# Optimization experiments

Measured on AMD Instinct MI355X. Metric: run time of the kernel, lower is better.

## Reference

```python
import jax, jax.numpy as jnp
import numpy as np

N_TOKENS = 100000
CUT = [0, 20000, 50000, 100000]  # cutoff_ends
D = 1024


def setup_inputs() -> dict:
    key = jax.random.key(0)
    ks = jax.random.split(key, 12)
    B, S = 2, 1024
    hidden = jax.random.normal(ks[0], (B, S, D), dtype=jnp.float32)
    target = jax.random.randint(ks[1], (B, S), 0, N_TOKENS, dtype=jnp.int64)
    s = 0.02
    # cluster 0 (shortlist) + cluster projection head
    w0 = jax.random.normal(ks[2], (20000, 1024), dtype=jnp.float32) * s
    b0 = jnp.zeros((20000,), jnp.float32)
    cluster_w = jax.random.normal(ks[3], (2, 1024), dtype=jnp.float32) * s  # n_clusters=2
    cluster_b = jnp.zeros((2,), jnp.float32)
    proj0 = jax.random.normal(ks[4], (1024, 1024), dtype=jnp.float32) * s  # d_proj x d_emb_0
    # tail cluster 1: d_emb_1 = 1024 // 4 = 256, vocab slice 20000..50000
    w1 = jax.random.normal(ks[5], (30000, 256), dtype=jnp.float32) * s
    b1 = jnp.zeros((30000,), jnp.float32)
    proj1 = jax.random.normal(ks[6], (1024, 256), dtype=jnp.float32) * s
    # tail cluster 2: d_emb_2 = 1024 // 16 = 64, vocab slice 50000..100000
    w2 = jax.random.normal(ks[7], (50000, 64), dtype=jnp.float32) * s
    b2 = jnp.zeros((50000,), jnp.float32)
    proj2 = jax.random.normal(ks[8], (1024, 64), dtype=jnp.float32) * s
    return {"hidden": hidden, "target": target,
            "w0": w0, "b0": b0, "cluster_w": cluster_w, "cluster_b": cluster_b, "proj0": proj0,
            "w1": w1, "b1": b1, "proj1": proj1,
            "w2": w2, "b2": b2, "proj2": proj2}


def reference(hidden, target, w0, b0, cluster_w, cluster_b, proj0,
              w1, b1, proj1, w2, b2, proj2):
    tgt_shape = target.shape
    h = hidden.reshape(-1, D)            # [N, d_proj]
    t = target.reshape(-1)               # [N]

    # head: shortlist logits + cluster logits, via low-rank projection
    head_w = jnp.concatenate([w0, cluster_w], axis=0)   # [20002, 1024]
    head_b = jnp.concatenate([b0, cluster_b], axis=0)
    head_logit = (h @ proj0) @ head_w.T + head_b        # [N, 20002]
    head_lp = jax.nn.log_softmax(head_logit, axis=1)

    nll = jnp.zeros(t.shape, h.dtype)

    # cluster 0 (shortlist): logprob is head_lp at the target id
    m0 = t < CUT[1]
    idx0 = jnp.clip(t, 0, CUT[1] - 1)
    lp0 = jnp.take_along_axis(head_lp, idx0[:, None], axis=1)[:, 0]
    nll = jnp.where(m0, -lp0, nll)

    # tail clusters. NOTE: faithful to original quirk head_logprob[:, -i]
    tails = [(CUT[1], CUT[2], w1, b1, proj1), (CUT[2], CUT[3], w2, b2, proj2)]
    for i, (left, right, w, b, p) in enumerate(tails, start=1):
        m = (t >= left) & (t < right)
        tail_logit = (h @ p) @ w.T + b                  # [N, right-left]
        tail_lp = jax.nn.log_softmax(tail_logit, axis=1)
        ti = jnp.clip(t - left, 0, right - left - 1)
        lp = head_lp[:, -i] + jnp.take_along_axis(tail_lp, ti[:, None], axis=1)[:, 0]
        nll = jnp.where(m, -lp, nll)

    return nll.reshape(tgt_shape)
```

## Files before the change

kernel.cpp:

```cpp
#include <hip/hip_runtime.h>
#include <cstdint>
#include <cstddef>

#define DEV static __device__ __forceinline__

typedef __attribute__((ext_vector_type(8))) short bf16x8_t;
typedef __attribute__((ext_vector_type(4))) float f32x4_t;

DEV unsigned short f2bf(float f) {
  union { float f; unsigned u; } v; v.f = f;
  unsigned r = v.u + 0x7fffu + ((v.u >> 16) & 1u);
  return (unsigned short)(r >> 16);
}

DEV void gl_lds16(const void* g, void* l) {
  __builtin_amdgcn_global_load_lds(
      (const __attribute__((address_space(1))) void*)g,
      (__attribute__((address_space(3))) void*)l,
      16, 0, 0);
}

__global__ __launch_bounds__(256)
void prep_k(const int* __restrict__ target,
            int* __restrict__ idx1, int* __restrict__ pos1,
            int* __restrict__ idx2, int* __restrict__ pos2,
            int* __restrict__ cnts,
            const float* __restrict__ p0, const float* __restrict__ p1,
            const float* __restrict__ p2, unsigned short* __restrict__ pAll,
            const float* __restrict__ s0, unsigned short* __restrict__ d0, int n0,
            const float* __restrict__ s1, unsigned short* __restrict__ d1, int n1,
            const float* __restrict__ s2, unsigned short* __restrict__ d2, int n2,
            const float* __restrict__ s3, unsigned short* __restrict__ d3, int n3,
            const float* __restrict__ s4, unsigned short* __restrict__ d4, int n4) {
  const int bid = blockIdx.x;
  const int tid = threadIdx.x;
  if (bid == 0) {
    __shared__ int c1, c2;
    if (tid == 0) { c1 = 0; c2 = 0; }
    __syncthreads();
    for (int i = tid; i < 2048; i += 256) {
      int t = target[i];
      if (t >= 20000 && t < 50000) {
        int p = atomicAdd(&c1, 1); idx1[p] = i; pos1[i] = p;
      } else if (t >= 50000) {
        int p = atomicAdd(&c2, 1); idx2[p] = i; pos2[i] = p;
      }
    }
    __syncthreads();
    if (tid == 0) { cnts[0] = c1; cnts[1] = c2; }
    return;
  }
  if (bid <= 1344) {
    __shared__ float tile[32][33];
    int b = bid - 1;
    const float* src; unsigned short* dst; int C, bx, by;
    if (b < 1024)      { src = p0; dst = pAll;               C = 1024; bx = b % 32; by = b / 32; }
    else if (b < 1280) { int q = b - 1024; src = p1; dst = pAll + 1024 * 1024; C = 256; bx = q % 8; by = q / 8; }
    else               { int q = b - 1280; src = p2; dst = pAll + 1280 * 1024; C = 64;  bx = q % 2; by = q / 2; }
    const int R = 1024;
    int tx = tid & 31, ty = tid >> 5;
    int c0 = bx * 32, r0 = by * 32;
    for (int yy = ty; yy < 32; yy += 8)
      tile[yy][tx] = src[(size_t)(r0 + yy) * C + (c0 + tx)];
    __syncthreads();
    for (int yy = ty; yy < 32; yy += 8)
      dst[(size_t)(c0 + yy) * R + (r0 + tx)] = f2bf(tile[tx][yy]);
    return;
  }
  int j = (bid - 1345) * 256 + tid;
  const float* s; unsigned short* d;
  if (j < n0) { s = s0; d = d0; }
  else { j -= n0;
    if (j < n1) { s = s1; d = d1; }
    else { j -= n1;
      if (j < n2) { s = s2; d = d2; }
      else { j -= n2;
        if (j < n3) { s = s3; d = d3; }
        else { j -= n3; if (j >= n4) return; s = s4; d = d4; }
      }
    }
  }
  float4 f = ((const float4*)s)[j];
  ushort4 o;
  o.x = f2bf(f.x); o.y = f2bf(f.y); o.z = f2bf(f.z); o.w = f2bf(f.w);
  ((ushort4*)d)[j] = o;
}

__global__ __launch_bounds__(256)
void proj_gemm_k(const unsigned short* __restrict__ A,
                 const unsigned short* __restrict__ W,
                 unsigned short* __restrict__ Cout) {
  __shared__ __align__(16) unsigned short As[128 * 32];
  __shared__ __align__(16) unsigned short Bs[128 * 32];
  const int K = 1024, V = 1344;
  const int tm = blockIdx.x, tn = blockIdx.y;
  const int m0 = tm * 128, n0 = tn * 128;
  const int tid = threadIdx.x, wid = tid >> 6, lane = tid & 63;
  const int quad = lane >> 4, l16 = lane & 15;
  const int wr = wid >> 1, wc = wid & 1;

  f32x4_t acc[4][4];
  const f32x4_t zero4 = {0.f, 0.f, 0.f, 0.f};
#pragma unroll
  for (int i = 0; i < 4; ++i)
#pragma unroll
    for (int j = 0; j < 4; ++j) acc[i][j] = zero4;

  const int srow = wid * 32 + (lane >> 2);
  const int skk  = (lane & 3) * 8;
  const unsigned short* Ap0 = A + (size_t)(m0 + srow) * K + skk;
  const unsigned short* Ap1 = A + (size_t)(m0 + srow + 16) * K + skk;
  int wrow0 = n0 + srow;      if (wrow0 > V - 1) wrow0 = V - 1;
  int wrow1 = n0 + srow + 16; if (wrow1 > V - 1) wrow1 = V - 1;
  const unsigned short* Wp0 = W + (size_t)wrow0 * K + skk;
  const unsigned short* Wp1 = W + (size_t)wrow1 * K + skk;
  unsigned short* Asw = As + wid * 1024;
  unsigned short* Bsw = Bs + wid * 1024;

  for (int k0 = 0; k0 < K; k0 += 32) {
    gl_lds16(Ap0, Asw);
    gl_lds16(Ap1, Asw + 512);
    gl_lds16(Wp0, Bsw);
    gl_lds16(Wp1, Bsw + 512);
    Ap0 += 32; Ap1 += 32; Wp0 += 32; Wp1 += 32;
    __syncthreads();
    bf16x8_t af[4], bfr[4];
#pragma unroll
    for (int i = 0; i < 4; ++i)
      af[i] = *(const bf16x8_t*)(As + (size_t)(wr * 64 + i * 16 + l16) * 32 + quad * 8);
#pragma unroll
    for (int j = 0; j < 4; ++j)
      bfr[j] = *(const bf16x8_t*)(Bs + (size_t)(wc * 64 + j * 16 + l16) * 32 + quad * 8);
#pragma unroll
    for (int i = 0; i < 4; ++i)
#pragma unroll
      for (int j = 0; j < 4; ++j)
        acc[i][j] = __builtin_amdgcn_mfma_f32_16x16x32_bf16(af[i], bfr[j], acc[i][j], 0, 0, 0);
    __syncthreads();
  }
#pragma unroll
  for (int i = 0; i < 4; ++i)
#pragma unroll
    for (int j = 0; j < 4; ++j) {
      const int n = n0 + wc * 64 + j * 16 + l16;
      if (n < V) {
#pragma unroll
        for (int r = 0; r < 4; ++r) {
          const int m = m0 + wr * 64 + i * 16 + quad * 4 + r;
          Cout[(size_t)m * V + n] = f2bf(acc[i][j][r]);
        }
      }
    }
}


#define SBAR() __builtin_amdgcn_s_barrier()

#define STA(BUF, HALF, KT)                                                    \
  {                                                                           \
    const unsigned short* g_ = aB0 + (size_t)(HALF) * (128 * 1344) + (KT) * 64; \
    char* d_ = (char*)SA[BUF][HALF] + ldsw;                                   \
    gl_lds16(g_, d_);                                                         \
    gl_lds16(g_ + 64 * 1344, d_ + 8192);                                      \
  }

#define STB(BUF, HALF, KT)                                                    \
  {                                                                           \
    char* d_ = (char*)SB[BUF][HALF] + ldsw;                                   \
    gl_lds16(bP##HALF##0 + (KT) * 64, d_);                                    \
    gl_lds16(bP##HALF##1 + (KT) * 64, d_ + 8192);                             \
  }

#define MMQ(mb, nb, BB)                                                       \
  {                                                                           \
    _Pragma("unroll") for (int mi = 0; mi < 4; ++mi) {                        \
      _Pragma("unroll") for (int nj = 0; nj < 2; ++nj) {                      \
        acc[(mb) + mi][(nb) + nj] = __builtin_amdgcn_mfma_f32_16x16x32_bf16(  \
            Af[0][mi], BB[0][nj], acc[(mb) + mi][(nb) + nj], 0, 0, 0);        \
        acc[(mb) + mi][(nb) + nj] = __builtin_amdgcn_mfma_f32_16x16x32_bf16(  \
            Af[1][mi], BB[1][nj], acc[(mb) + mi][(nb) + nj], 0, 0, 0);        \
      }                                                                       \
    }                                                                         \
  }

#define PH(D_, E_, KTV)                                                       \
  {                                                                           \
    const int kt_ = (KTV);                                                    \
    const int t1_ = (kt_ + 1 > 15) ? 15 : (kt_ + 1);                          \
    const int t2_ = (kt_ + 2 > 15) ? 15 : (kt_ + 2);                          \
              \
    _Pragma("unroll") for (int mi = 0; mi < 4; ++mi) {                        \
      Af[0][mi] = *(const bf16x8_t*)(pa##D_##a + mi * 2048);                  \
      Af[1][mi] = *(const bf16x8_t*)(pa##D_##b + mi * 2048);                  \
    }                                                                         \
    _Pragma("unroll") for (int nj = 0; nj < 2; ++nj) {                        \
      Bh[0][nj] = *(const bf16x8_t*)(pb##D_##a + (2 + nj) * 2048);            \
      Bh[1][nj] = *(const bf16x8_t*)(pb##D_##b + (2 + nj) * 2048);            \
    }                                                                         \
    STB(E_, 1, t1_);                                                          \
    __builtin_amdgcn_s_setprio(1); MMQ(0, 0, Bl); __builtin_amdgcn_s_setprio(0); \
    SBAR();                                                                   \
              \
    __builtin_amdgcn_s_setprio(1); MMQ(0, 2, Bh); __builtin_amdgcn_s_setprio(0); \
    _Pragma("unroll") for (int mi = 0; mi < 4; ++mi) {                        \
      Af[0][mi] = *(const bf16x8_t*)(pa##D_##a + (4 + mi) * 2048);            \
      Af[1][mi] = *(const bf16x8_t*)(pa##D_##b + (4 + mi) * 2048);            \
    }                                                                         \
    STA(E_, 1, t1_);                                                          \
    SBAR();                                                                   \
               \
    STB(D_, 0, t2_);                                                          \
    __builtin_amdgcn_s_setprio(1); MMQ(4, 0, Bl); __builtin_amdgcn_s_setprio(0); \
    asm volatile("s_waitcnt vmcnt(2)" ::: "memory");                          \
    SBAR();                                                                   \
           \
    STA(D_, 0, t2_);                                                          \
    _Pragma("unroll") for (int nj = 0; nj < 2; ++nj) {                        \
      Bl[0][nj] = *(const bf16x8_t*)(pb##E_##a + nj * 2048);                  \
      Bl[1][nj] = *(const bf16x8_t*)(pb##E_##b + nj * 2048);                  \
    }                                                                         \
    __builtin_amdgcn_s_setprio(1); MMQ(4, 2, Bh); __builtin_amdgcn_s_setprio(0); \
    SBAR();                                                                   \
  }

#define PROLOGUE6()                                                           \
  { STB(0, 0, 0); STA(0, 0, 0); STB(0, 1, 0); STA(0, 1, 0);                   \
    STB(1, 0, 1); STA(1, 0, 1); }

typedef unsigned short lds_half_t[2][8192];

DEV void head_body(char* UB, int bid,
                   const unsigned short* __restrict__ Pall,
                   const unsigned short* __restrict__ w0b,
                   const float* __restrict__ b0, const float* __restrict__ cb,
                   float* __restrict__ part0, float* __restrict__ g0,
                   float* __restrict__ cg, const int* __restrict__ target) {
  lds_half_t* SA = (lds_half_t*)UB;
  lds_half_t* SB = (lds_half_t*)(UB + 65536);

  const int V = 20002;
  const int orig = (bid & 7) * 79 + (bid >> 3);
  const int mt = orig & 7, stripe = orig >> 3;
  const int m0 = mt * 256, n0 = stripe * 256;

  const int tid = threadIdx.x;
  const int wid = tid >> 6, lane = tid & 63;
  const int quad = lane >> 4, l16 = lane & 15;
  const int wr = wid >> 2, wc = wid & 3;

  const int r0  = tid >> 3;
  const int ibh = ((tid & 7) ^ (r0 & 7)) << 3;

  const unsigned short* aB0 = Pall + (size_t)(m0 + r0) * 1344 + ibh;
  int br00 = n0 + r0;            if (br00 > V - 1) br00 = V - 1;
  int br01 = n0 + r0 + 64;       if (br01 > V - 1) br01 = V - 1;
  int br10 = n0 + 128 + r0;      if (br10 > V - 1) br10 = V - 1;
  int br11 = n0 + 128 + r0 + 64; if (br11 > V - 1) br11 = V - 1;
  const unsigned short* bP00 = w0b + (size_t)br00 * 1024 + ibh;
  const unsigned short* bP01 = w0b + (size_t)br01 * 1024 + ibh;
  const unsigned short* bP10 = w0b + (size_t)br10 * 1024 + ibh;
  const unsigned short* bP11 = w0b + (size_t)br11 * 1024 + ibh;

  const int ldsw = wid * 1024;

  const int aoff0 = l16 * 128 + ((quad ^ (l16 & 3)) << 4) + (((l16 >> 2) & 1) << 6);
  const int aoff1 = aoff0 ^ 64;
  const char* pa0a = (const char*)SA[0][wr] + aoff0;
  const char* pa0b = (const char*)SA[0][wr] + aoff1;
  const char* pa1a = (const char*)SA[1][wr] + aoff0;
  const char* pa1b = (const char*)SA[1][wr] + aoff1;
  const char* pb0a = (const char*)SB[0][wc >> 1] + (wc & 1) * 8192 + aoff0;
  const char* pb0b = (const char*)SB[0][wc >> 1] + (wc & 1) * 8192 + aoff1;
  const char* pb1a = (const char*)SB[1][wc >> 1] + (wc & 1) * 8192 + aoff0;
  const char* pb1b = (const char*)SB[1][wc >> 1] + (wc & 1) * 8192 + aoff1;

  f32x4_t acc[8][4];
  const f32x4_t zero4 = {0.f, 0.f, 0.f, 0.f};
#pragma unroll
  for (int i = 0; i < 8; ++i)
#pragma unroll
    for (int j = 0; j < 4; ++j) acc[i][j] = zero4;

  bf16x8_t Af[2][4];
  bf16x8_t Bl[2][2];
  bf16x8_t Bh[2][2];

  PROLOGUE6();
  asm volatile("s_waitcnt vmcnt(4)" ::: "memory");
  SBAR();
#pragma unroll
  for (int nj = 0; nj < 2; ++nj) {
    Bl[0][nj] = *(const bf16x8_t*)(pb0a + nj * 2048);
    Bl[1][nj] = *(const bf16x8_t*)(pb0b + nj * 2048);
  }

#pragma unroll 1
  for (int ktp = 0; ktp < 8; ++ktp) {
    const int kt0 = 2 * ktp;
    PH(0, 1, kt0);
    PH(1, 0, kt0 + 1);
  }

  asm volatile("s_waitcnt vmcnt(0) lgkmcnt(0)" ::: "memory");
  SBAR();

  int nj[4]; float bj[4];
#pragma unroll
  for (int j = 0; j < 4; ++j) {
    nj[j] = n0 + wc * 64 + j * 16 + l16;
    bj[j] = (nj[j] < 20000) ? b0[nj[j]] : ((nj[j] < V) ? cb[nj[j] - 20000] : 0.f);
  }
  float* redf = (float*)UB;
#pragma unroll
  for (int i = 0; i < 8; ++i) {
#pragma unroll
    for (int r = 0; r < 4; ++r) {
      const int rloc = i * 16 + quad * 4 + r;
      const int token = m0 + wr * 128 + rloc;
      float v[4], sum = 0.f;
#pragma unroll
      for (int j = 0; j < 4; ++j) {
        v[j] = acc[i][j][r] + bj[j];
        if (nj[j] < V) sum += __expf(v[j]);
      }
#pragma unroll
      for (int off = 1; off < 16; off <<= 1)
        sum += __shfl_xor(sum, off, 64);
      if (l16 == 0) redf[(wr * 4 + wc) * 128 + rloc] = sum;
      const int t = target[token];
      const int gi = (t < 19999) ? t : 19999;
#pragma unroll
      for (int j = 0; j < 4; ++j) {
        if (nj[j] == gi) g0[token] = v[j];
        if (nj[j] == 20000) cg[2 * token]     = v[j];
        if (nj[j] == 20001) cg[2 * token + 1] = v[j];
      }
    }
  }
  __syncthreads();
  if (tid < 256) {
    const int wrr = tid >> 7, rr = tid & 127;
    const float s = redf[(wrr * 4 + 0) * 128 + rr] + redf[(wrr * 4 + 1) * 128 + rr]
                  + redf[(wrr * 4 + 2) * 128 + rr] + redf[(wrr * 4 + 3) * 128 + rr];
    part0[(size_t)(m0 + tid) * 79 + stripe] = s;
  }
}

#undef PH
#undef MMQ
#undef STA
#undef STB
#undef PROLOGUE6
#undef SBAR

template <int KT>
DEV void tail_body(char* UB, int tn,
                   const unsigned short* __restrict__ A, int ldA,
                   const unsigned short* __restrict__ W,
                   const float* __restrict__ bias, int V, int ntiles,
                   const int* __restrict__ rowidx,
                   const int* __restrict__ cnt_ptr,
                   float* __restrict__ partials,
                   float* __restrict__ gathered,
                   const int* __restrict__ target, int glo) {
  constexpr int NC = KT / 32;
  unsigned short (*Ws)[128 * 32] = (unsigned short (*)[128 * 32])UB;
  unsigned short (*As)[128 * 32] = (unsigned short (*)[128 * 32])(UB + NC * 8192);
  float (*red)[128] = (float (*)[128])(UB + 2 * NC * 8192);

  const int n0 = tn * 128;
  const int Meff = *cnt_ptr;
  const int tid = threadIdx.x;
  const bool act = tid < 256;
  const int wid = tid >> 6, lane = tid & 63;
  const int quad = lane >> 4, l16 = lane & 15;
  const int wr = wid >> 1, wc = wid & 1;
  const int srow = wid * 32 + (lane >> 2);
  const int skk  = (lane & 3) * 8;

  int wrow0 = n0 + srow;      if (wrow0 > V - 1) wrow0 = V - 1;
  int wrow1 = n0 + srow + 16; if (wrow1 > V - 1) wrow1 = V - 1;
  if (act) {
#pragma unroll
    for (int c = 0; c < NC; ++c) {
      gl_lds16(W + (size_t)wrow0 * KT + c * 32 + skk, Ws[c] + wid * 1024);
      gl_lds16(W + (size_t)wrow1 * KT + c * 32 + skk, Ws[c] + wid * 1024 + 512);
    }
  }

  int nj[4]; float bj[4];
#pragma unroll
  for (int j = 0; j < 4; ++j) {
    nj[j] = n0 + wc * 64 + j * 16 + l16;
    bj[j] = (act && nj[j] < V) ? bias[nj[j]] : 0.f;
  }

  const int nm = (Meff + 127) >> 7;
  for (int m = 0; m < nm; ++m) {
    const int m0 = m * 128;
    if (act) {
      int ar0 = m0 + srow;      if (ar0 > Meff - 1) ar0 = Meff - 1;
      int ar1 = m0 + srow + 16; if (ar1 > Meff - 1) ar1 = Meff - 1;
      ar0 = rowidx[ar0]; ar1 = rowidx[ar1];
#pragma unroll
      for (int c = 0; c < NC; ++c) {
        gl_lds16(A + (size_t)ar0 * ldA + c * 32 + skk, As[c] + wid * 1024);
        gl_lds16(A + (size_t)ar1 * ldA + c * 32 + skk, As[c] + wid * 1024 + 512);
      }
    }
    __syncthreads();

    if (act) {
      f32x4_t acc[4][4];
      const f32x4_t zero4 = {0.f, 0.f, 0.f, 0.f};
#pragma unroll
      for (int i = 0; i < 4; ++i)
#pragma unroll
        for (int j = 0; j < 4; ++j) acc[i][j] = zero4;
#pragma unroll
      for (int c = 0; c < NC; ++c) {
        bf16x8_t af[4], bfr[4];
#pragma unroll
        for (int i = 0; i < 4; ++i)
          af[i] = *(const bf16x8_t*)(As[c] + (size_t)(wr * 64 + i * 16 + l16) * 32 + quad * 8);
#pragma unroll
        for (int j = 0; j < 4; ++j)
          bfr[j] = *(const bf16x8_t*)(Ws[c] + (size_t)(wc * 64 + j * 16 + l16) * 32 + quad * 8);
#pragma unroll
        for (int i = 0; i < 4; ++i)
#pragma unroll
          for (int j = 0; j < 4; ++j)
            acc[i][j] = __builtin_amdgcn_mfma_f32_16x16x32_bf16(af[i], bfr[j], acc[i][j], 0, 0, 0);
      }

#pragma unroll
      for (int i = 0; i < 4; ++i) {
#pragma unroll
        for (int r = 0; r < 4; ++r) {
          const int row = wr * 64 + i * 16 + quad * 4 + r;
          const int gr = m0 + row;
          const int grc = (gr < Meff) ? gr : (Meff - 1);
          const int token = rowidx[grc];
          float v[4], sum = 0.f;
#pragma unroll
          for (int j = 0; j < 4; ++j) {
            v[j] = acc[i][j][r] + bj[j];
            if (nj[j] < V) sum += __expf(v[j]);
          }
#pragma unroll
          for (int off = 1; off < 16; off <<= 1)
            sum += __shfl_xor(sum, off, 64);
          if (l16 == 0) red[wc][row] = sum;
          const int gi = target[token] - glo;
#pragma unroll
          for (int j = 0; j < 4; ++j)
            if (nj[j] == gi) gathered[token] = v[j];
        }
      }
    }
    __syncthreads();
    if (tid < 128 && (m0 + tid) < Meff)
      partials[(size_t)(m0 + tid) * ntiles + tn] = red[0][tid] + red[1][tid];
  }
}

__global__ __launch_bounds__(512, 2)
void fused_k(const unsigned short* __restrict__ Pall,
             const unsigned short* __restrict__ w0b,
             const float* __restrict__ b0, const float* __restrict__ cb,
             float* __restrict__ part0, float* __restrict__ g0,
             float* __restrict__ cg, const int* __restrict__ target,
             const unsigned short* __restrict__ w1b, const float* __restrict__ b1,
             const int* __restrict__ idx1, const int* __restrict__ cnt1,
             float* __restrict__ part1, float* __restrict__ g1,
             const unsigned short* __restrict__ w2b, const float* __restrict__ b2,
             const int* __restrict__ idx2, const int* __restrict__ cnt2,
             float* __restrict__ part2, float* __restrict__ g2,
             int nt1, int nt2) {
  __shared__ __align__(16) char UB[132096];
  const int bid = blockIdx.x;
  if (bid < 632) {
    head_body(UB, bid, Pall, w0b, b0, cb, part0, g0, cg, target);
  } else if (bid < 632 + 235) {
    tail_body<256>(UB, bid - 632, Pall + 1024, 1344, w1b, b1, 30000, nt1,
                   idx1, cnt1, part1, g1, target, 20000);
  } else {
    tail_body<64>(UB, bid - 867, Pall + 1280, 1344, w2b, b2, 50000, nt2,
                  idx2, cnt2, part2, g2, target, 50000);
  }
}

__global__ __launch_bounds__(256)
void combine_k(const float* __restrict__ part0,
               const float* __restrict__ part1, int nt1,
               const float* __restrict__ part2, int nt2,
               const float* __restrict__ g0, const float* __restrict__ g1,
               const float* __restrict__ g2, const float* __restrict__ cg,
               const int* __restrict__ pos1, const int* __restrict__ pos2,
               const int* __restrict__ target, float* __restrict__ out) {
  const int w = threadIdx.x >> 6, lane = threadIdx.x & 63;
  const int token = blockIdx.x * 4 + w;
  const int t = target[token];

  float S = 0.f;
  for (int i = lane; i < 79; i += 64)
    S += part0[(size_t)token * 79 + i];
#pragma unroll
  for (int off = 1; off < 64; off <<= 1)
    S += __shfl_xor(S, off, 64);
  const float lse_head = __logf(S);

  float res;
  if (t < 20000) {
    res = lse_head - g0[token];
  } else {
    const float* pt; int nt; float gv, ch; int row;
    if (t < 50000) { pt = part1; nt = nt1; gv = g1[token]; ch = cg[2 * token + 1]; row = pos1[token]; }
    else           { pt = part2; nt = nt2; gv = g2[token]; ch = cg[2 * token];     row = pos2[token]; }
    float S2 = 0.f;
    for (int i = lane; i < nt; i += 64)
      S2 += pt[(size_t)row * nt + i];
#pragma unroll
    for (int off = 1; off < 64; off <<= 1)
      S2 += __shfl_xor(S2, off, 64);
    float lse_t = __logf(S2);
    res = -((ch - lse_head) + (gv - lse_t));
  }
  if (lane == 0) out[token] = res;
}

extern "C" void kernel_launch(void* const* d_in, const int* in_sizes, int n_in,
                              void* d_out, int out_size, void* d_ws, size_t ws_size,
                              hipStream_t stream) {
  (void)in_sizes; (void)n_in; (void)out_size; (void)ws_size;
  const float* hidden = (const float*)d_in[0];
  const int*   target = (const int*)d_in[1];
  const float* w0     = (const float*)d_in[2];
  const float* b0     = (const float*)d_in[3];
  const float* cw     = (const float*)d_in[4];
  const float* cb     = (const float*)d_in[5];
  const float* proj0  = (const float*)d_in[6];
  const float* w1     = (const float*)d_in[7];
  const float* b1     = (const float*)d_in[8];
  const float* proj1  = (const float*)d_in[9];
  const float* w2     = (const float*)d_in[10];
  const float* b2     = (const float*)d_in[11];
  const float* proj2  = (const float*)d_in[12];
  float* out = (float*)d_out;

  const int NT1 = 235, NT2 = 391;

  char* p = (char*)d_ws;
  auto alloc = [&](size_t bytes) {
    char* r = p; p += (bytes + 255) & ~(size_t)255; return r;
  };
  unsigned short* Hb   = (unsigned short*)alloc(2048ull * 1024 * 2);
  unsigned short* pAll = (unsigned short*)alloc(1344ull * 1024 * 2);
  unsigned short* w0b  = (unsigned short*)alloc(20002ull * 1024 * 2);
  unsigned short* w1b  = (unsigned short*)alloc(30000ull * 256 * 2);
  unsigned short* w2b  = (unsigned short*)alloc(50000ull * 64 * 2);
  unsigned short* Pall = (unsigned short*)alloc(2048ull * 1344 * 2);
  float* part0 = (float*)alloc(2048ull * 79 * 4);
  float* part1 = (float*)alloc(2048ull * NT1 * 4);
  float* part2 = (float*)alloc(2048ull * NT2 * 4);
  float* g0 = (float*)alloc(2048 * 4);
  float* g1 = (float*)alloc(2048 * 4);
  float* g2 = (float*)alloc(2048 * 4);
  float* cg = (float*)alloc(2048 * 2 * 4);
  int* idx1 = (int*)alloc(2048 * 4);
  int* pos1 = (int*)alloc(2048 * 4);
  int* idx2 = (int*)alloc(2048 * 4);
  int* pos2 = (int*)alloc(2048 * 4);
  int* cnts = (int*)alloc(2 * 4);

  const int c_h = 2048 * 1024 / 4, c_w0 = 20000 * 1024 / 4, c_cw = 2048 / 4,
            c_w1 = 30000 * 256 / 4, c_w2 = 50000 * 64 / 4;
  const int ctot = c_h + c_w0 + c_cw + c_w1 + c_w2;
  const int nb_cast = (ctot + 255) / 256;
  prep_k<<<1 + 1344 + nb_cast, 256, 0, stream>>>(
      target, idx1, pos1, idx2, pos2, cnts,
      proj0, proj1, proj2, pAll,
      hidden, Hb, c_h,
      w0, w0b, c_w0,
      cw, w0b + 20000ull * 1024, c_cw,
      w1, w1b, c_w1,
      w2, w2b, c_w2);

  proj_gemm_k<<<dim3(16, 11), 256, 0, stream>>>(Hb, pAll, Pall);

  fused_k<<<632 + NT1 + NT2, 512, 0, stream>>>(
      Pall, w0b, b0, cb, part0, g0, cg, target,
      w1b, b1, idx1, cnts + 0, part1, g1,
      w2b, b2, idx2, cnts + 1, part2, g2,
      NT1, NT2);

  combine_k<<<512, 256, 0, stream>>>(part0, part1, NT1, part2, NT2,
      g0, g1, g2, cg, pos1, pos2, target, out);
}
```

Baseline: 418.3 us.

## Use all 8 waves in tail GEMM with double-buffered A staging and 256-row tiles

```diff
diff --git a/kernel.cpp b/kernel.cpp
--- a/kernel.cpp
+++ b/kernel.cpp
@@ -354,91 +354,100 @@
 #undef SBAR
 
 template <int KT>
-DEV void tail_body(char* UB, int tn,
-                   const unsigned short* __restrict__ A, int ldA,
-                   const unsigned short* __restrict__ W,
-                   const float* __restrict__ bias, int V, int ntiles,
-                   const int* __restrict__ rowidx,
-                   const int* __restrict__ cnt_ptr,
-                   float* __restrict__ partials,
-                   float* __restrict__ gathered,
-                   const int* __restrict__ target, int glo) {
-  constexpr int NC = KT / 32;
-  unsigned short (*Ws)[128 * 32] = (unsigned short (*)[128 * 32])UB;
-  unsigned short (*As)[128 * 32] = (unsigned short (*)[128 * 32])(UB + NC * 8192);
-  float (*red)[128] = (float (*)[128])(UB + 2 * NC * 8192);
+DEV void tail_body8(char* UB, int tn,
+                    const unsigned short* __restrict__ A, int ldA,
+                    const unsigned short* __restrict__ W,
+                    const float* __restrict__ bias, int V, int nt2x,
+                    const int* __restrict__ rowidx,
+                    const int* __restrict__ cnt_ptr,
+                    float* __restrict__ partials,
+                    float* __restrict__ gathered,
+                    const int* __restrict__ target, int glo) {
+  constexpr int KC  = KT / 64;
+  constexpr int NCB = KT / 32;
+  unsigned short* Bs = (unsigned short*)UB;
+  char* AsB = UB + NCB * 8192;
 
   const int n0 = tn * 128;
   const int Meff = *cnt_ptr;
   const int tid = threadIdx.x;
-  const bool act = tid < 256;
-  const int wid = tid >> 6, lane = tid & 63;
+  const int lane = tid & 63, wid = tid >> 6;
   const int quad = lane >> 4, l16 = lane & 15;
   const int wr = wid >> 1, wc = wid & 1;
-  const int srow = wid * 32 + (lane >> 2);
-  const int skk  = (lane & 3) * 8;
-
-  int wrow0 = n0 + srow;      if (wrow0 > V - 1) wrow0 = V - 1;
-  int wrow1 = n0 + srow + 16; if (wrow1 > V - 1) wrow1 = V - 1;
-  if (act) {
-#pragma unroll
-    for (int c = 0; c < NC; ++c) {
-      gl_lds16(W + (size_t)wrow0 * KT + c * 32 + skk, Ws[c] + wid * 1024);
-      gl_lds16(W + (size_t)wrow1 * KT + c * 32 + skk, Ws[c] + wid * 1024 + 512);
-    }
-  }
+  const int srow = tid >> 2;
+  const int scol = (tid & 3) * 8;
+  const int ldsw = wid * 1024;
+
+  int wrow = n0 + srow; if (wrow > V - 1) wrow = V - 1;
+#pragma unroll
+  for (int c = 0; c < NCB; ++c)
+    gl_lds16(W + (size_t)wrow * KT + c * 32 + scol, (char*)Bs + c * 8192 + ldsw);
 
   int nj[4]; float bj[4];
 #pragma unroll
   for (int j = 0; j < 4; ++j) {
     nj[j] = n0 + wc * 64 + j * 16 + l16;
-    bj[j] = (act && nj[j] < V) ? bias[nj[j]] : 0.f;
-  }
-
-  const int nm = (Meff + 127) >> 7;
-  for (int m = 0; m < nm; ++m) {
-    const int m0 = m * 128;
-    if (act) {
-      int ar0 = m0 + srow;      if (ar0 > Meff - 1) ar0 = Meff - 1;
-      int ar1 = m0 + srow + 16; if (ar1 > Meff - 1) ar1 = Meff - 1;
-      ar0 = rowidx[ar0]; ar1 = rowidx[ar1];
-#pragma unroll
-      for (int c = 0; c < NC; ++c) {
-        gl_lds16(A + (size_t)ar0 * ldA + c * 32 + skk, As[c] + wid * 1024);
-        gl_lds16(A + (size_t)ar1 * ldA + c * 32 + skk, As[c] + wid * 1024 + 512);
+    bj[j] = (nj[j] < V) ? bias[nj[j]] : 0.f;
+  }
+
+  const int nm = (Meff + 255) >> 8;
+  const int S = nm * KC;
+
+  auto stageA = [&](int s, int buf) {
+    const int m = s / KC, k = s - m * KC;
+#pragma unroll
+    for (int cc = 0; cc < 2; ++cc)
+#pragma unroll
+      for (int h = 0; h < 2; ++h) {
+        int ar = m * 256 + srow + h * 128;
+        if (ar > Meff - 1) ar = Meff - 1;
+        if (ar < 0) ar = 0;
+        const int Arow = rowidx[ar];
+        gl_lds16(A + (size_t)Arow * ldA + k * 64 + cc * 32 + scol,
+                 AsB + buf * 32768 + cc * 16384 + h * 8192 + ldsw);
       }
+  };
+
+  stageA(0, 0);
+  __syncthreads();
+
+  f32x4_t acc[4][4];
+  const f32x4_t zero4 = {0.f, 0.f, 0.f, 0.f};
+
+  for (int s = 0; s < S; ++s) {
+    const int buf = s & 1;
+    const int m = s / KC, k = s - m * KC;
+    if (s + 1 < S) stageA(s + 1, buf ^ 1);
+    if (k == 0) {
+#pragma unroll
+      for (int i = 0; i < 4; ++i)
+#pragma unroll
+        for (int j = 0; j < 4; ++j) acc[i][j] = zero4;
     }
-    __syncthreads();
-
-    if (act) {
-      f32x4_t acc[4][4];
-      const f32x4_t zero4 = {0.f, 0.f, 0.f, 0.f};
+#pragma unroll
+    for (int cc = 0; cc < 2; ++cc) {
+      bf16x8_t af[4], bfr[4];
 #pragma unroll
       for (int i = 0; i < 4; ++i)
-#pragma unroll
-        for (int j = 0; j < 4; ++j) acc[i][j] = zero4;
-#pragma unroll
-      for (int c = 0; c < NC; ++c) {
-        bf16x8_t af[4], bfr[4];
-#pragma unroll
-        for (int i = 0; i < 4; ++i)
-          af[i] = *(const bf16x8_t*)(As[c] + (size_t)(wr * 64 + i * 16 + l16) * 32 + quad * 8);
+        af[i] = *(const bf16x8_t*)(AsB + buf * 32768 + cc * 16384 +
+                                   (wr * 64 + i * 16 + l16) * 64 + quad * 16);
+#pragma unroll
+      for (int j = 0; j < 4; ++j)
+        bfr[j] = *(const bf16x8_t*)((char*)Bs + (k * 2 + cc) * 8192 +
+                                    (wc * 64 + j * 16 + l16) * 64 + quad * 16);
+#pragma unroll
+      for (int i = 0; i < 4; ++i)
 #pragma unroll
         for (int j = 0; j < 4; ++j)
-          bfr[j] = *(const bf16x8_t*)(Ws[c] + (size_t)(wc * 64 + j * 16 + l16) * 32 + quad * 8);
-#pragma unroll
-        for (int i = 0; i < 4; ++i)
-#pragma unroll
-          for (int j = 0; j < 4; ++j)
-            acc[i][j] = __builtin_amdgcn_mfma_f32_16x16x32_bf16(af[i], bfr[j], acc[i][j], 0, 0, 0);
-      }
-
+          acc[i][j] = __builtin_amdgcn_mfma_f32_16x16x32_bf16(af[i], bfr[j], acc[i][j], 0, 0, 0);
+    }
+    if (k == KC - 1) {
 #pragma unroll
       for (int i = 0; i < 4; ++i) {
 #pragma unroll
         for (int r = 0; r < 4; ++r) {
           const int row = wr * 64 + i * 16 + quad * 4 + r;
-          const int gr = m0 + row;
+          const int gr = m * 256 + row;
           const int grc = (gr < Meff) ? gr : (Meff - 1);
           const int token = rowidx[grc];
           float v[4], sum = 0.f;
@@ -450,7 +459,8 @@
 #pragma unroll
           for (int off = 1; off < 16; off <<= 1)
             sum += __shfl_xor(sum, off, 64);
-          if (l16 == 0) red[wc][row] = sum;
+          if (l16 == 0)
+            partials[(size_t)grc * nt2x + 2 * tn + wc] = sum;
           const int gi = target[token] - glo;
 #pragma unroll
           for (int j = 0; j < 4; ++j)
@@ -459,8 +469,6 @@
       }
     }
     __syncthreads();
-    if (tid < 128 && (m0 + tid) < Meff)
-      partials[(size_t)(m0 + tid) * ntiles + tn] = red[0][tid] + red[1][tid];
   }
 }
 
@@ -476,17 +484,17 @@
              const unsigned short* __restrict__ w2b, const float* __restrict__ b2,
              const int* __restrict__ idx2, const int* __restrict__ cnt2,
              float* __restrict__ part2, float* __restrict__ g2,
-             int nt1, int nt2) {
+             int nt1x2, int nt2x2) {
   __shared__ __align__(16) char UB[132096];
   const int bid = blockIdx.x;
   if (bid < 632) {
     head_body(UB, bid, Pall, w0b, b0, cb, part0, g0, cg, target);
   } else if (bid < 632 + 235) {
-    tail_body<256>(UB, bid - 632, Pall + 1024, 1344, w1b, b1, 30000, nt1,
-                   idx1, cnt1, part1, g1, target, 20000);
+    tail_body8<256>(UB, bid - 632, Pall + 1024, 1344, w1b, b1, 30000, nt1x2,
+                    idx1, cnt1, part1, g1, target, 20000);
   } else {
-    tail_body<64>(UB, bid - 867, Pall + 1280, 1344, w2b, b2, 50000, nt2,
-                  idx2, cnt2, part2, g2, target, 50000);
+    tail_body8<64>(UB, bid - 867, Pall + 1280, 1344, w2b, b2, 50000, nt2x2,
+                   idx2, cnt2, part2, g2, target, 50000);
   }
 }
 
@@ -549,6 +557,7 @@
   float* out = (float*)d_out;
 
   const int NT1 = 235, NT2 = 391;
+  const int NT1X = 2 * NT1, NT2X = 2 * NT2;
 
   char* p = (char*)d_ws;
   auto alloc = [&](size_t bytes) {
@@ -561,8 +570,8 @@
   unsigned short* w2b  = (unsigned short*)alloc(50000ull * 64 * 2);
   unsigned short* Pall = (unsigned short*)alloc(2048ull * 1344 * 2);
   float* part0 = (float*)alloc(2048ull * 79 * 4);
-  float* part1 = (float*)alloc(2048ull * NT1 * 4);
-  float* part2 = (float*)alloc(2048ull * NT2 * 4);
+  float* part1 = (float*)alloc(2048ull * NT1X * 4);
+  float* part2 = (float*)alloc(2048ull * NT2X * 4);
   float* g0 = (float*)alloc(2048 * 4);
   float* g1 = (float*)alloc(2048 * 4);
   float* g2 = (float*)alloc(2048 * 4);
@@ -592,8 +601,8 @@
       Pall, w0b, b0, cb, part0, g0, cg, target,
       w1b, b1, idx1, cnts + 0, part1, g1,
       w2b, b2, idx2, cnts + 1, part2, g2,
-      NT1, NT2);
-
-  combine_k<<<512, 256, 0, stream>>>(part0, part1, NT1, part2, NT2,
+      NT1X, NT2X);
+
+  combine_k<<<512, 256, 0, stream>>>(part0, part1, NT1X, part2, NT2X,
       g0, g1, g2, cg, pos1, pos2, target, out);
 }
```

After: 384.2 us. 8.2% less time.
